# Kernel optimization log

Hardware: AMD Instinct MI355X
Metric: run time of the kernel (lower is better)

## Reference

```python
import jax, jax.numpy as jnp
import numpy as np
from jax import lax

ALPHA = 0.5       # DYS step size (init kwarg alpha)
SV_THRESH = 1e-6  # pinv singular-value threshold (init kwarg sv_thresh)
TOL = 1e-2        # convergence tolerance (forward default tol=0.01)


def _build_matrices(A):
    # A: (batch, m, n).  Standard-form matrix A_std = [A, -A, I_m]: (batch, m, N), N = 2n+m.
    batch, m, n = A.shape
    I_m = jnp.eye(m, dtype=A.dtype)
    A_std = jnp.concatenate([A, -A, jnp.broadcast_to(I_m, (batch, m, m))], axis=2)
    # M maps z -> u: (n, N) = [I_n, -I_n, 0]
    M = jnp.concatenate([jnp.eye(n, dtype=A.dtype), -jnp.eye(n, dtype=A.dtype),
                         jnp.zeros((n, m), dtype=A.dtype)], axis=1)
    AAt = A_std @ jnp.swapaxes(A_std, -2, -1)              # (batch, m, m)
    U, S, _ = jnp.linalg.svd(AAt)
    S_inv = jnp.where(S > SV_THRESH, 1.0 / S, jnp.zeros_like(S))
    AAt_pinv = (U * S_inv[..., None, :]) @ jnp.swapaxes(U, -2, -1)
    P_perp = jnp.swapaxes(A_std, -2, -1) @ AAt_pinv        # (batch, N, m)
    return A_std, M, P_perp


def _apply_T(z, u_nom, A_std, M, P_perp, b2):
    # One Davis-Yin splitting step. z: (batch, N), b2: (batch, m)
    x = jnp.maximum(z, 0.0)                                # proj_C2
    grad = (x @ M.T - u_nom) @ M                           # (batch, N)
    v = 2.0 * x - z - ALPHA * grad
    resid = jnp.einsum('bmN,bN->bm', A_std, v) - b2
    y = v - jnp.einsum('bNm,bm->bN', P_perp, resid)        # proj_C1
    return z + y - x


def setup_inputs() -> dict:
    key = jax.random.key(0)
    k1, k2, k3 = jax.random.split(key, 3)
    batch, m, n = 8192, 32, 16
    u_nom = jax.random.normal(k1, (batch, n), dtype=jnp.float32)
    A = jax.random.normal(k2, (batch, m, n), dtype=jnp.float32)
    b = jax.random.uniform(k3, (batch, m, 1), dtype=jnp.float32)
    return {"u_nom": u_nom, "A": A, "b": b, "max_iter": 100}


def reference(u_nom, A, b, max_iter):
    A_std, M, P_perp = _build_matrices(A)
    b2 = b[..., 0]
    batch = u_nom.shape[0]
    N = M.shape[1]
    z0 = jnp.zeros((batch, N), dtype=u_nom.dtype)

    # JFB: run to convergence (max_iter-1 steps, on-device residual check) ...
    def cond(state):
        k, z, res = state
        return jnp.logical_and(res >= TOL, k < max_iter - 1)

    def body(state):
        k, z, _ = state
        z_new = _apply_T(z, u_nom, A_std, M, P_perp, b2)
        return k + 1, z_new, jnp.max(jnp.abs(z_new - z))

    _, z, _ = lax.while_loop(cond, body, (0, z0, jnp.array(jnp.inf, dtype=u_nom.dtype)))

    # ... then one final T step (n_grad_iters=1)
    z_star = _apply_T(z, u_nom, A_std, M, P_perp, b2)
    u_star = z_star @ M.T
    return u_star, z_star
```

## Files before the change

kernel.cpp:

```cpp
#include <hip/hip_runtime.h>
#include <stdint.h>

#define TOL 1e-2f
#define WPB 4
#define WS_CTL_OFF 192
#define WS_Z_OFF   4096

__device__ __forceinline__ float bcastf(float v, int l) {
    return __int_as_float(__builtin_amdgcn_readlane(__float_as_int(v), l));
}

template <int PAT>
__device__ __forceinline__ float swz(float v) {
    return __int_as_float(__builtin_amdgcn_ds_swizzle(__float_as_int(v), PAT));
}
#define SWZ_XOR16 0x401F

template <int MODE>
__global__ __launch_bounds__(256) __attribute__((amdgpu_waves_per_eu(1)))
void dys_pass(
    const float* __restrict__ u_nom,
    const float* __restrict__ Amat,
    const float* __restrict__ bvec,
    const int*   __restrict__ mi_ptr,
    const int*   __restrict__ ctl,
    unsigned long long* __restrict__ flags,
    float*       __restrict__ zstore,
    int zcap,
    float*       __restrict__ out,
    int B)
{
    if (MODE == 1) { if (ctl[1]) return; }

    const int tid   = threadIdx.x;
    const int lane  = tid & 63;
    const int wib   = tid >> 6;
    const int elem  = blockIdx.x * WPB + wib;
    const int row32 = lane & 31;
    const int col16 = lane & 15;

    __shared__ __align__(16) float ldsT[WPB][32 * 17];
    float* T = ldsT[wib];

    const float* Ab = Amat + (size_t)elem * 512 + (size_t)row32 * 16;
    float A_row[16];
    {
        float4 a0 = ((const float4*)Ab)[0];
        float4 a1 = ((const float4*)Ab)[1];
        float4 a2 = ((const float4*)Ab)[2];
        float4 a3 = ((const float4*)Ab)[3];
        A_row[0]=a0.x;  A_row[1]=a0.y;  A_row[2]=a0.z;  A_row[3]=a0.w;
        A_row[4]=a1.x;  A_row[5]=a1.y;  A_row[6]=a1.z;  A_row[7]=a1.w;
        A_row[8]=a2.x;  A_row[9]=a2.y;  A_row[10]=a2.z; A_row[11]=a2.w;
        A_row[12]=a3.x; A_row[13]=a3.y; A_row[14]=a3.z; A_row[15]=a3.w;
    }
    if (lane < 32) {
        #pragma unroll
        for (int k = 0; k < 16; ++k) T[row32 * 17 + k] = A_row[k];
    }
    const float un = u_nom[(size_t)elem * 16 + col16];
    const float bv = bvec[(size_t)elem * 32 + row32];

    float W[48];

    {
        float A2[16];
        #pragma unroll
        for (int k = 0; k < 16; ++k) A2[k] = A_row[k] + A_row[k];
        #pragma unroll
        for (int j = 0; j < 32; ++j) {
            float acc = (row32 == j) ? 1.f : 0.f;
            #pragma unroll
            for (int k = 0; k < 16; ++k)
                acc = fmaf(A2[k], bcastf(A_row[k], j), acc);
            W[16 + j] = acc;
        }
    }

    #pragma unroll
    for (int p = 0; p < 32; ++p) {
        float piv = bcastf(W[16 + p], p);
        float d = __builtin_amdgcn_rcpf(piv);
        d = d * (2.f - piv * d);
        float g = W[16 + p] * d;
        g = (row32 == p) ? (1.f - d) : g;
        float negg = -g;
        #pragma unroll
        for (int j = 0; j < 32; ++j) {
            if (j == p) continue;
            float spj = bcastf(W[16 + j], p);
            W[16 + j] = fmaf(negg, spj, W[16 + j]);
        }
        W[16 + p] = (row32 == p) ? d : negg;
    }

    #pragma unroll
    for (int k = 0; k < 16; ++k) W[k] = 0.f;
    #pragma unroll
    for (int m = 0; m < 32; ++m) {
        float q = W[16 + m];
        #pragma unroll
        for (int k = 0; k < 16; ++k)
            W[k] = fmaf(q, bcastf(A_row[k], m), W[k]);
    }

    float tq[16];
    #pragma unroll
    for (int k = 0; k < 16; ++k) tq[k] = 0.f;
    #pragma unroll
    for (int m = 0; m < 32; ++m) {
        float a_mi = T[m * 17 + col16];
        #pragma unroll
        for (int k = 0; k < 16; ++k)
            tq[k] = fmaf(a_mi, bcastf(W[k], m), tq[k]);
    }

    if (lane < 32) {
        #pragma unroll
        for (int k = 0; k < 16; ++k) T[row32 * 17 + k] = W[k];
    }
    if (lane < 32) {
        #pragma unroll
        for (int m = 0; m < 32; ++m) W[16 + m] = T[m * 17 + col16];
        #pragma unroll
        for (int k = 0; k < 16; ++k) W[k] = tq[k];
    }

    float cneg;
    {
        float c0 = 0.f, c1 = 0.f;
        #pragma unroll
        for (int m = 0; m < 32; m += 2) {
            c0 = fmaf(W[16 + m], bcastf(bv, m),     c0);
            c1 = fmaf(W[17 + m], bcastf(bv, m + 1), c1);
        }
        cneg = -(c0 + c1);
    }

    const float sgn  = (lane >= 16 && lane < 32) ? 1.f : -1.f;
    const float sgn0 = (lane & 16) ? -1.f : 1.f;
    const float nun  = -un;
    const int pslot = (lane < 16) ? lane : ((lane < 32) ? (32 + lane) : (lane - 16));

    const int mi = *mi_ptr;
    const int nsteps = (MODE == 0) ? mi : ctl[0];

    float* zp = zstore + (size_t)elem * 64 + lane;
    const size_t zstride = (size_t)B * 64;

    float z = 0.f;
    unsigned long long m0 = 0ull, m1 = 0ull, b0 = 1ull, b1 = 0ull;

    const float4* Pv = (const float4*)T;

    for (int k = 1; k <= nsteps; ++k) {
        float z16 = swz<SWZ_XOR16>(z);
        float x   = fmaxf(z, 0.f);
        float x16 = fmaxf(z16, 0.f);
        float t1  = x - x16;
        float s   = (t1 - (z - z16)) + un;
        float h   = fmaf(2.f, x, -z);

        T[pslot] = (lane < 32) ? s : h;
        float ee = fmaf(sgn0, t1, nun);

        float acc0 = cneg, acc1 = 0.f, acc2 = 0.f, acc3 = 0.f;
        #pragma unroll
        for (int q = 0; q < 12; ++q) {
            float4 p = Pv[q];
            acc0 = fmaf(W[4*q+0], p.x, acc0);
            acc1 = fmaf(W[4*q+1], p.y, acc1);
            acc2 = fmaf(W[4*q+2], p.z, acc2);
            acc3 = fmaf(W[4*q+3], p.w, acc3);
        }
        float acc = (acc0 + acc1) + (acc2 + acc3);

        float t    = (lane < 32) ? fmaf(0.5f, ee, acc) : acc;
        float znew = fmaf(sgn, t, x);

        if (MODE == 0) {
            unsigned long long cy = b0 >> 63;
            b0 <<= 1; b1 = (b1 << 1) | cy;
            unsigned long long any = __ballot(fabsf(znew - z) >= TOL);
            if (any) { m0 |= b0; m1 |= b1; }
            if (k <= zcap) { *zp = znew; zp += zstride; }
        }
        z = znew;
    }

    if (MODE == 0) {
        if (lane == 0) {
            int slot = blockIdx.x & 7;
            atomicOr(flags + 2 * slot,     m0);
            atomicOr(flags + 2 * slot + 1, m1);
        }
    } else {
        float z16b = swz<SWZ_XOR16>(z);
        if (lane < 16) out[(size_t)elem * 16 + lane] = z - z16b;
        out[(size_t)B * 16 + (size_t)elem * 64 + lane] = z;
    }
}

__global__ void dys_reduce(const int* __restrict__ mi_ptr,
                           const unsigned long long* __restrict__ flags,
                           int zcap, int* __restrict__ ctl)
{
    if (threadIdx.x != 0) return;
    unsigned long long m0 = 0ull, m1 = 0ull;
    for (int s = 0; s < 8; ++s) { m0 |= flags[2*s]; m1 |= flags[2*s+1]; }
    int mi = *mi_ptr;
    int S = mi;
    for (int k = 1; k < mi && k < 128; ++k) {
        unsigned long long bit = (k < 64) ? ((m0 >> k) & 1ull)
                                          : ((m1 >> (k - 64)) & 1ull);
        if (!bit) { S = k + 1; break; }
    }
    if (S < 1) S = 1;
    ctl[0] = S;
    ctl[1] = (S <= zcap) ? 1 : 0;
}

__global__ __launch_bounds__(256) void dys_gather(
    const int* __restrict__ ctl, const float* __restrict__ zstore,
    float* __restrict__ out, int B)
{
    if (!ctl[1]) return;
    int tid  = blockIdx.x * 256 + threadIdx.x;
    int lane = tid & 63;
    int elem = tid >> 6;
    int S = ctl[0];
    float z = zstore[(size_t)(S - 1) * B * 64 + (size_t)elem * 64 + lane];
    float z16 = swz<SWZ_XOR16>(z);
    if (lane < 16) out[(size_t)elem * 16 + lane] = z - z16;
    out[(size_t)B * 16 + (size_t)elem * 64 + lane] = z;
}

extern "C" void kernel_launch(void* const* d_in, const int* in_sizes, int n_in,
                              void* d_out, int out_size, void* d_ws, size_t ws_size,
                              hipStream_t stream) {
    (void)n_in; (void)out_size;
    const float* u_nom = (const float*)d_in[0];
    const float* Amat  = (const float*)d_in[1];
    const float* bvec  = (const float*)d_in[2];
    const int*   mi    = (const int*)d_in[3];

    const int B = in_sizes[0] / 16;

    unsigned long long* flags = (unsigned long long*)d_ws;
    int* ctl = (int*)((char*)d_ws + WS_CTL_OFF);
    float* zstore = (float*)((char*)d_ws + WS_Z_OFF);

    const size_t stepBytes = (size_t)B * 64 * sizeof(float);
    int zcap = 0;
    if (ws_size > WS_Z_OFF + stepBytes)
        zcap = (int)((ws_size - WS_Z_OFF) / stepBytes);
    if (zcap > 127) zcap = 127;

    hipMemsetAsync(d_ws, 0, 256, stream);

    const int blocks = B / WPB;
    dys_pass<0><<<blocks, 64 * WPB, 0, stream>>>(u_nom, Amat, bvec, mi, ctl,
                                                 flags, zstore, zcap, (float*)d_out, B);
    dys_reduce<<<1, 64, 0, stream>>>(mi, flags, zcap, ctl);
    dys_pass<1><<<blocks, 64 * WPB, 0, stream>>>(u_nom, Amat, bvec, mi, ctl,
                                                 flags, zstore, zcap, (float*)d_out, B);
    dys_gather<<<B * 64 / 256, 256, 0, stream>>>(ctl, zstore, (float*)d_out, B);
}
```

Baseline: 284.8 us.

## Replace 32x32 pseudo-inverse with 16x16 Woodbury inverse in setup

```diff
diff --git a/kernel.cpp b/kernel.cpp
--- a/kernel.cpp
+++ b/kernel.cpp
@@ -5,6 +5,8 @@
 #define WPB 4
 #define WS_CTL_OFF 192
 #define WS_Z_OFF   4096
+
+#define LDSW 768
 
 __device__ __forceinline__ float bcastf(float v, int l) {
     return __int_as_float(__builtin_amdgcn_readlane(__float_as_int(v), l));
@@ -39,91 +41,119 @@
     const int row32 = lane & 31;
     const int col16 = lane & 15;
 
-    __shared__ __align__(16) float ldsT[WPB][32 * 17];
+    __shared__ __align__(16) float ldsT[WPB][LDSW];
     float* T = ldsT[wib];
 
     const float* Ab = Amat + (size_t)elem * 512 + (size_t)row32 * 16;
     float A_row[16];
+    float4 a0, a1, a2, a3;
     {
-        float4 a0 = ((const float4*)Ab)[0];
-        float4 a1 = ((const float4*)Ab)[1];
-        float4 a2 = ((const float4*)Ab)[2];
-        float4 a3 = ((const float4*)Ab)[3];
+        a0 = ((const float4*)Ab)[0];
+        a1 = ((const float4*)Ab)[1];
+        a2 = ((const float4*)Ab)[2];
+        a3 = ((const float4*)Ab)[3];
         A_row[0]=a0.x;  A_row[1]=a0.y;  A_row[2]=a0.z;  A_row[3]=a0.w;
         A_row[4]=a1.x;  A_row[5]=a1.y;  A_row[6]=a1.z;  A_row[7]=a1.w;
         A_row[8]=a2.x;  A_row[9]=a2.y;  A_row[10]=a2.z; A_row[11]=a2.w;
         A_row[12]=a3.x; A_row[13]=a3.y; A_row[14]=a3.z; A_row[15]=a3.w;
     }
     if (lane < 32) {
-        #pragma unroll
-        for (int k = 0; k < 16; ++k) T[row32 * 17 + k] = A_row[k];
+        float4* Td = (float4*)(T + row32 * 16);
+        Td[0] = a0; Td[1] = a1; Td[2] = a2; Td[3] = a3;
     }
     const float un = u_nom[(size_t)elem * 16 + col16];
     const float bv = bvec[(size_t)elem * 32 + row32];
 
-    float W[48];
-
-    {
-        float A2[16];
-        #pragma unroll
-        for (int k = 0; k < 16; ++k) A2[k] = A_row[k] + A_row[k];
-        #pragma unroll
-        for (int j = 0; j < 32; ++j) {
-            float acc = (row32 == j) ? 1.f : 0.f;
-            #pragma unroll
-            for (int k = 0; k < 16; ++k)
-                acc = fmaf(A2[k], bcastf(A_row[k], j), acc);
-            W[16 + j] = acc;
-        }
-    }
-
-    #pragma unroll
-    for (int p = 0; p < 32; ++p) {
-        float piv = bcastf(W[16 + p], p);
+
+    float P[16];
+    #pragma unroll
+    for (int j = 0; j < 16; ++j) P[j] = (j == col16) ? 1.f : 0.f;
+    #pragma unroll
+    for (int m = 0; m < 32; ++m) {
+        float am  = T[m * 16 + col16];
+        float am2 = am + am;
+        const float4* Rm = (const float4*)(T + m * 16);
+        #pragma unroll
+        for (int q = 0; q < 4; ++q) {
+            float4 r = Rm[q];
+            P[4*q+0] = fmaf(am2, r.x, P[4*q+0]);
+            P[4*q+1] = fmaf(am2, r.y, P[4*q+1]);
+            P[4*q+2] = fmaf(am2, r.z, P[4*q+2]);
+            P[4*q+3] = fmaf(am2, r.w, P[4*q+3]);
+        }
+    }
+
+    #pragma unroll
+    for (int p = 0; p < 16; ++p) {
+        float piv = bcastf(P[p], p);
         float d = __builtin_amdgcn_rcpf(piv);
         d = d * (2.f - piv * d);
-        float g = W[16 + p] * d;
-        g = (row32 == p) ? (1.f - d) : g;
+        float g = P[p] * d;
+        g = (col16 == p) ? (1.f - d) : g;
         float negg = -g;
         #pragma unroll
-        for (int j = 0; j < 32; ++j) {
+        for (int j = 0; j < 16; ++j) {
             if (j == p) continue;
-            float spj = bcastf(W[16 + j], p);
-            W[16 + j] = fmaf(negg, spj, W[16 + j]);
-        }
-        W[16 + p] = (row32 == p) ? d : negg;
-    }
-
+            float spj = bcastf(P[j], p);
+            P[j] = fmaf(negg, spj, P[j]);
+        }
+        P[p] = (col16 == p) ? d : negg;
+    }
+
+    if (lane < 16) {
+        float4* Gd = (float4*)(T + 512 + col16 * 16);
+        Gd[0] = make_float4(P[0],  P[1],  P[2],  P[3]);
+        Gd[1] = make_float4(P[4],  P[5],  P[6],  P[7]);
+        Gd[2] = make_float4(P[8],  P[9],  P[10], P[11]);
+        Gd[3] = make_float4(P[12], P[13], P[14], P[15]);
+    }
+
+    float W[48];
     #pragma unroll
     for (int k = 0; k < 16; ++k) W[k] = 0.f;
     #pragma unroll
-    for (int m = 0; m < 32; ++m) {
-        float q = W[16 + m];
+    for (int t = 0; t < 16; ++t) {
+        float at = A_row[t];
+        const float4* Gt = (const float4*)(T + 512 + t * 16);
+        #pragma unroll
+        for (int q = 0; q < 4; ++q) {
+            float4 r = Gt[q];
+            W[4*q+0] = fmaf(at, r.x, W[4*q+0]);
+            W[4*q+1] = fmaf(at, r.y, W[4*q+1]);
+            W[4*q+2] = fmaf(at, r.z, W[4*q+2]);
+            W[4*q+3] = fmaf(at, r.w, W[4*q+3]);
+        }
+    }
+
+    float v[16];
+    #pragma unroll
+    for (int k = 0; k < 16; ++k) v[k] = (lane < 32) ? P[k] : W[k];
+
+    if (lane < 32) {
         #pragma unroll
         for (int k = 0; k < 16; ++k)
-            W[k] = fmaf(q, bcastf(A_row[k], m), W[k]);
-    }
-
-    float tq[16];
-    #pragma unroll
-    for (int k = 0; k < 16; ++k) tq[k] = 0.f;
-    #pragma unroll
-    for (int m = 0; m < 32; ++m) {
-        float a_mi = T[m * 17 + col16];
-        #pragma unroll
-        for (int k = 0; k < 16; ++k)
-            tq[k] = fmaf(a_mi, bcastf(W[k], m), tq[k]);
-    }
-
-    if (lane < 32) {
-        #pragma unroll
-        for (int k = 0; k < 16; ++k) T[row32 * 17 + k] = W[k];
-    }
-    if (lane < 32) {
-        #pragma unroll
-        for (int m = 0; m < 32; ++m) W[16 + m] = T[m * 17 + col16];
-        #pragma unroll
-        for (int k = 0; k < 16; ++k) W[k] = tq[k];
+            W[k] = fmaf(P[k], -0.5f, (k == col16) ? 0.5f : 0.f);
+    }
+
+    {
+        const bool low = (lane < 32);
+        #pragma unroll
+        for (int m = 0; m < 32; ++m) {
+            const float4* Rm = (const float4*)(T + m * 16);
+            float c0 = 0.f, c1 = 0.f, c2 = 0.f, c3 = 0.f;
+            #pragma unroll
+            for (int q = 0; q < 4; ++q) {
+                float4 r = Rm[q];
+                c0 = fmaf(v[4*q+0], r.x, c0);
+                c1 = fmaf(v[4*q+1], r.y, c1);
+                c2 = fmaf(v[4*q+2], r.z, c2);
+                c3 = fmaf(v[4*q+3], r.w, c3);
+            }
+            float c = (c0 + c1) + (c2 + c3);
+            float dsel = (m == row32) ? 1.f : 0.f;
+            float up = fmaf(-2.f, c, dsel);
+            W[16 + m] = low ? c : up;
+        }
     }
 
     float cneg;
@@ -137,16 +167,18 @@
         cneg = -(c0 + c1);
     }
 
-    const float sgn  = (lane >= 16 && lane < 32) ? 1.f : -1.f;
-    const float sgn0 = (lane & 16) ? -1.f : 1.f;
-    const float nun  = -un;
+    const float sgn   = (lane >= 16 && lane < 32) ? 1.f : -1.f;
+    const float sgn0  = (lane & 16) ? -1.f : 1.f;
+    const float nun   = -un;
+    const float half0 = (lane < 32) ? 0.5f : 0.f;
     const int pslot = (lane < 16) ? lane : ((lane < 32) ? (32 + lane) : (lane - 16));
 
     const int mi = *mi_ptr;
     const int nsteps = (MODE == 0) ? mi : ctl[0];
 
-    float* zp = zstore + (size_t)elem * 64 + lane;
-    const size_t zstride = (size_t)B * 64;
+    const uint32_t zoff = (uint32_t)elem * 64u + (uint32_t)lane;
+    float* zbase = zstore;
+    const size_t zstrideE = (size_t)B * 64;
 
     float z = 0.f;
     unsigned long long m0 = 0ull, m1 = 0ull, b0 = 1ull, b1 = 0ull;
@@ -175,7 +207,7 @@
         }
         float acc = (acc0 + acc1) + (acc2 + acc3);
 
-        float t    = (lane < 32) ? fmaf(0.5f, ee, acc) : acc;
+        float t    = fmaf(half0, ee, acc);
         float znew = fmaf(sgn, t, x);
 
         if (MODE == 0) {
@@ -183,7 +215,7 @@
             b0 <<= 1; b1 = (b1 << 1) | cy;
             unsigned long long any = __ballot(fabsf(znew - z) >= TOL);
             if (any) { m0 |= b0; m1 |= b1; }
-            if (k <= zcap) { *zp = znew; zp += zstride; }
+            if (k <= zcap) { zbase[zoff] = znew; zbase += zstrideE; }
         }
         z = znew;
     }
```

Result: faster. 268.3 us (-5.8%).
